# Kernel optimization log

Measured on AMD Instinct MI355X. Metric: run time of the kernel, lower is better.

## Reference

```python
import jax, jax.numpy as jnp
import numpy as np

EPS = 1e-5
NEG_SLOPE = 0.1


def setup_inputs() -> dict:
    key = jax.random.key(0)
    ks = jax.random.split(key, 4)
    B, Cin, Cout, D, E, EMB = 2, 32, 32, 40, 3, 1
    return {
        "x": jax.random.normal(ks[0], (B, Cin, D, D, D), dtype=jnp.float32),
        "embedding": jax.random.normal(ks[1], (B, EMB), dtype=jnp.float32),
        "route_w": jax.random.normal(ks[2], (EMB, E), dtype=jnp.float32),
        "route_b": jnp.zeros((E,), dtype=jnp.float32),
        "expert_kernels": jax.random.normal(ks[3], (E, Cout, Cin, 3, 3, 3), dtype=jnp.float32) * 0.05,
        "expert_bias": jnp.zeros((E, Cout), dtype=jnp.float32),
        "gamma": jnp.ones((Cout,), dtype=jnp.float32),
        "beta": jnp.zeros((Cout,), dtype=jnp.float32),
    }


def reference(x, embedding, route_w, route_b, expert_kernels, expert_bias, gamma, beta):
    # CondConv routing: sigmoid(Linear(embedding)) -> per-sample expert weights [B, E]
    r = jax.nn.sigmoid(embedding @ route_w + route_b)
    # Per-sample combined kernel [B, O, I, 3, 3, 3] and bias [B, O]
    w = jnp.einsum('be,eoixyz->boixyz', r, expert_kernels)
    b = r @ expert_bias

    def conv_one(xi, wi):
        # xi: [Cin, D, H, W], wi: [O, I, 3, 3, 3] -> [Cout, D, H, W]
        return jax.lax.conv_general_dilated(
            xi[None], wi, window_strides=(1, 1, 1), padding='SAME',
            dimension_numbers=('NCDHW', 'OIDHW', 'NCDHW'))[0]

    y = jax.vmap(conv_one)(x, w) + b[:, :, None, None, None]  # [B, O, D, H, W]

    # BatchNorm3d (training mode: biased batch stats over B,D,H,W per channel)
    mean = jnp.mean(y, axis=(0, 2, 3, 4), keepdims=True)
    var = jnp.mean(jnp.square(y - mean), axis=(0, 2, 3, 4), keepdims=True)
    y = (y - mean) * jax.lax.rsqrt(var + EPS)
    y = y * gamma[None, :, None, None, None] + beta[None, :, None, None, None]

    # LeakyReLU(0.1)
    y = jnp.where(y >= 0, y, NEG_SLOPE * y)

    # Upsample nearest, scale_factor=2 on all 3 spatial dims
    y = jnp.repeat(jnp.repeat(jnp.repeat(y, 2, axis=2), 2, axis=3), 2, axis=4)
    return y
```

## Files before the change

### kernel.cpp

```cpp
#include <hip/hip_runtime.h>
#include <hip/hip_bf16.h>
#include <math.h>

#define BB   2
#define CIN  32
#define COUT 32
#define DM   40
#define PD   42
#define NPTS (DM*DM)
#define NVOL (DM*DM*DM)
#define EPSBN 1e-5f
#define NSLOT 64

typedef short  bf16x8  __attribute__((ext_vector_type(8)));
typedef short  bf16x4  __attribute__((ext_vector_type(4)));
typedef float  floatx4 __attribute__((ext_vector_type(4)));

#define WS_WFRAG 0
#define WS_BCOMB 27648
#define WS_SUM2  27712
#define WS_XPAD2 31808
#define WS_Y     2402624

#define REPACK_BLOCKS (PD*PD*BB)
#define NW_ELEMS  (2*2*27*64*8)
#define PREP_ELEMS (NW_ELEMS + 64 + NSLOT*64)
#define PREP_BLOCKS ((PREP_ELEMS + 255) / 256)

static __device__ __forceinline__ short f2bf(float f) {
    __hip_bfloat16 h = __float2bfloat16(f);
    return *reinterpret_cast<short*>(&h);
}
static __device__ __forceinline__ float bf2f(short s) {
    union { unsigned u; float f; } cv;
    cv.u = ((unsigned)(unsigned short)s) << 16;
    return cv.f;
}

__global__ void prep_repack_kernel(const float* __restrict__ x,
                                   const float* __restrict__ emb,
                                   const float* __restrict__ rw,
                                   const float* __restrict__ rb,
                                   const float* __restrict__ ek,
                                   const float* __restrict__ ebias,
                                   float* __restrict__ ws) {
    __shared__ __hip_bfloat16 tile[PD * 32];
    const int bid = blockIdx.x;
    const int t = threadIdx.x;
    if (bid < REPACK_BLOCKS) {
        int b  = bid / (PD * PD);
        int r  = bid % (PD * PD);
        int zp = r / PD, yp = r % PD;
        __hip_bfloat16* row = (__hip_bfloat16*)(ws + WS_XPAD2) +
                              ((((size_t)b * PD + zp) * PD + yp) * PD) * 32;
        const bool inz = (zp >= 1 && zp <= DM && yp >= 1 && yp <= DM);
        const int i  = t >> 3;
        const int xl = t & 7;
        #pragma unroll
        for (int k = 0; k < 6; ++k) {
            int xp = xl + 8 * k;
            if (xp < PD) {
                float v = 0.0f;
                if (inz && xp >= 1 && xp <= DM)
                    v = x[(size_t)(b * CIN + i) * NVOL +
                          (zp - 1) * NPTS + (yp - 1) * DM + (xp - 1)];
                tile[xp * 32 + i] = __float2bfloat16(v);
            }
        }
        __syncthreads();
        const unsigned* ts = (const unsigned*)tile;
        unsigned* rowu = (unsigned*)row;
        for (int j = t; j < PD * 32 / 2; j += 256) rowu[j] = ts[j];
        return;
    }
    int idx = (bid - REPACK_BLOCKS) * 256 + t;
    __hip_bfloat16* wfrag = (__hip_bfloat16*)(ws + WS_WFRAG);
    if (idx < NW_ELEMS) {
        int j    = idx & 7;
        int lane = (idx >> 3) & 63;
        int tap  = (idx >> 9) % 27;
        int nt   = (idx / (27 * 512)) & 1;
        int b    = idx / (2 * 27 * 512);
        int o = nt * 16 + (lane & 15);
        int i = (lane >> 4) * 8 + j;
        float e0 = emb[b];
        float w = 0.0f;
        #pragma unroll
        for (int e = 0; e < 3; ++e) {
            float r = 1.0f / (1.0f + expf(-(e0 * rw[e] + rb[e])));
            w += r * ek[((e * COUT + o) * CIN + i) * 27 + tap];
        }
        wfrag[idx] = __float2bfloat16(w);
    } else if (idx < NW_ELEMS + 64) {
        int j2 = idx - NW_ELEMS;
        int b = j2 >> 5, o = j2 & 31;
        float e0 = emb[b];
        float bv = 0.0f;
        #pragma unroll
        for (int e = 0; e < 3; ++e) {
            float r = 1.0f / (1.0f + expf(-(e0 * rw[e] + rb[e])));
            bv += r * ebias[e * COUT + o];
        }
        ws[WS_BCOMB + j2] = bv;
    } else if (idx < PREP_ELEMS) {
        ws[WS_SUM2 + (idx - NW_ELEMS - 64)] = 0.0f;
    }
}

__global__ __launch_bounds__(256, 8) void conv_mfma_kernel(
        const __hip_bfloat16* __restrict__ xp2,
        const bf16x8* __restrict__ wfrag,
        const float* __restrict__ bcomb,
        __hip_bfloat16* __restrict__ y,
        float* __restrict__ sums2) {
    const int g   = blockIdx.x & 7;
    const int s   = blockIdx.x >> 3;
    const int b   = s / 125;
    const int rem = s % 125;
    const int z   = g * 5 + rem / 25;
    const int mc  = rem % 25;

    const int tid = threadIdx.x, lane = tid & 63, wv = tid >> 6;
    const int mt = wv & 1, nt = wv >> 1;
    const int quad = lane >> 4, l15 = lane & 15;

    __shared__ float lstat[64];
    __shared__ short ytile[32 * 72];
    __shared__ short atile[5 * PD * 32];

    if (tid < 64) lstat[tid] = 0.0f;

    const int y0  = (mc * 64) / DM;
    const int pa0 = mc * 64 + mt * 32 + l15;
    const int pa1 = pa0 + 16;
    const int ya0 = pa0 / DM, xa0 = pa0 % DM;
    const int ya1 = pa1 / DM, xa1 = pa1 % DM;
    const int af0 = ((ya0 - y0) * PD + xa0) * 32 + quad * 8;
    const int af1 = ((ya1 - y0) * PD + xa1) * 32 + quad * 8;

    const bf16x8* wbase = wfrag + ((b * 2 + nt) * 27) * 64 + lane;
    const int nrows = min(5, PD - y0);
    const int nchunk = nrows * (PD * 32 / 8);

    floatx4 acc0 = {0.f, 0.f, 0.f, 0.f};
    floatx4 acc1 = {0.f, 0.f, 0.f, 0.f};

    for (int dz = 0; dz < 3; ++dz) {
        __syncthreads();
        {
            const bf16x8* src = (const bf16x8*)(xp2 +
                ((((size_t)b * PD + (z + dz)) * PD + y0) * PD) * 32);
            bf16x8* dst = (bf16x8*)atile;
            for (int j = tid; j < nchunk; j += 256) dst[j] = src[j];
        }
        __syncthreads();
        #pragma unroll
        for (int t9 = 0; t9 < 9; ++t9) {
            const int dy = t9 / 3, dx = t9 % 3;
            const int aoff = (dy * PD + dx) * 32;
            bf16x8 av0 = *(const bf16x8*)&atile[af0 + aoff];
            bf16x8 av1 = *(const bf16x8*)&atile[af1 + aoff];
            bf16x8 bv  = wbase[(dz * 9 + t9) * 64];
            acc0 = __builtin_amdgcn_mfma_f32_16x16x32_bf16(av0, bv, acc0, 0, 0, 0);
            acc1 = __builtin_amdgcn_mfma_f32_16x16x32_bf16(av1, bv, acc1, 0, 0, 0);
        }
    }

    const int o = nt * 16 + l15;
    const float bias = bcomb[b * COUT + o];

    float u0 = acc0[0] + bias, u1 = acc0[1] + bias;
    float u2 = acc0[2] + bias, u3 = acc0[3] + bias;
    float w0 = acc1[0] + bias, w1 = acc1[1] + bias;
    float w2 = acc1[2] + bias, w3 = acc1[3] + bias;

    {
        const int s0 = mt * 32 + quad * 4;
        bf16x4 p0 = { f2bf(u0), f2bf(u1), f2bf(u2), f2bf(u3) };
        bf16x4 p1 = { f2bf(w0), f2bf(w1), f2bf(w2), f2bf(w3) };
        *(bf16x4*)&ytile[o * 72 + s0]      = p0;
        *(bf16x4*)&ytile[o * 72 + s0 + 16] = p1;
    }

    float vs = u0 + u1 + u2 + u3 + w0 + w1 + w2 + w3;
    float vq = u0*u0 + u1*u1 + u2*u2 + u3*u3 + w0*w0 + w1*w1 + w2*w2 + w3*w3;
    vs += __shfl_xor(vs, 16); vq += __shfl_xor(vq, 16);
    vs += __shfl_xor(vs, 32); vq += __shfl_xor(vq, 32);
    if (lane < 16) {
        atomicAdd(&lstat[o],      vs);
        atomicAdd(&lstat[32 + o], vq);
    }
    __syncthreads();

    {
        const int o2 = tid >> 3, c = tid & 7;
        bf16x8 v = *(const bf16x8*)&ytile[o2 * 72 + c * 8];
        __hip_bfloat16* dst = y + ((size_t)(b * COUT + o2) * DM + z) * NPTS
                            + mc * 64 + c * 8;
        *(bf16x8*)dst = v;
    }
    if (tid < 64) {
        int slot = ((b * DM + z) * 25 + mc) & (NSLOT - 1);
        atomicAdd(&sums2[slot * 64 + tid], lstat[tid]);
    }
}

__global__ __launch_bounds__(256) void upsample_kernel(
        const __hip_bfloat16* __restrict__ yin,
        const float* __restrict__ sums2,
        const float* __restrict__ gamma,
        const float* __restrict__ beta,
        float* __restrict__ out) {
    __shared__ float partl[4][64];
    __shared__ float ssc[32], ssh[32];
    __shared__ float fplane[NPTS];
    const int tid = threadIdx.x;
    const int cc  = blockIdx.x / DM;
    const int z   = blockIdx.x % DM;
    const int c   = cc & 31;

    {
        int sg = tid >> 6, st = tid & 63;
        float p = 0.0f;
        #pragma unroll
        for (int s = 0; s < 16; ++s) p += sums2[(sg * 16 + s) * 64 + st];
        partl[sg][st] = p;
    }
    __syncthreads();
    if (tid < 64) {
        partl[0][tid] += partl[1][tid] + partl[2][tid] + partl[3][tid];
    }
    __syncthreads();
    if (tid < 32) {
        const float invN = 1.0f / (float)(BB * NVOL);
        float mean  = partl[0][tid] * invN;
        float var   = partl[0][32 + tid] * invN - mean * mean;
        float scale = gamma[tid] * rsqrtf(var + EPSBN);
        ssc[tid] = scale;
        ssh[tid] = beta[tid] - mean * scale;
    }
    __syncthreads();

    const float sc = ssc[c], sh = ssh[c];
    if (tid < NPTS / 8) {
        bf16x8 rv = *(const bf16x8*)(yin + ((size_t)cc * DM + z) * NPTS + tid * 8);
        #pragma unroll
        for (int j = 0; j < 8; ++j) {
            float v = bf2f(rv[j]) * sc + sh;
            fplane[tid * 8 + j] = (v >= 0.0f) ? v : 0.1f * v;
        }
    }
    __syncthreads();

    float* outp = out + ((size_t)cc * 80 + 2 * z) * 6400;
    #pragma unroll 2
    for (int cch = tid; cch < 2 * 1600; cch += 256) {
        int plane = cch / 1600;
        int cp    = cch - plane * 1600;
        int yy2   = cp / 20;
        int sx0   = (cp % 20) * 2;
        const float* srow = fplane + (yy2 >> 1) * DM;
        float v0 = srow[sx0], v1 = srow[sx0 + 1];
        floatx4 q = {v0, v0, v1, v1};
        *(floatx4*)(outp + (size_t)plane * 6400 + cp * 4) = q;
    }
}

extern "C" void kernel_launch(void* const* d_in, const int* in_sizes, int n_in,
                              void* d_out, int out_size, void* d_ws, size_t ws_size,
                              hipStream_t stream) {
    const float* x     = (const float*)d_in[0];
    const float* emb   = (const float*)d_in[1];
    const float* rw    = (const float*)d_in[2];
    const float* rb    = (const float*)d_in[3];
    const float* ek    = (const float*)d_in[4];
    const float* ebias = (const float*)d_in[5];
    const float* gamma = (const float*)d_in[6];
    const float* beta  = (const float*)d_in[7];
    float* ws  = (float*)d_ws;
    float* out = (float*)d_out;

    prep_repack_kernel<<<REPACK_BLOCKS + PREP_BLOCKS, 256, 0, stream>>>(
        x, emb, rw, rb, ek, ebias, ws);

    conv_mfma_kernel<<<2000, 256, 0, stream>>>(
        (const __hip_bfloat16*)(ws + WS_XPAD2), (const bf16x8*)(ws + WS_WFRAG),
        ws + WS_BCOMB, (__hip_bfloat16*)(ws + WS_Y), ws + WS_SUM2);

    upsample_kernel<<<BB * COUT * DM, 256, 0, stream>>>(
        (const __hip_bfloat16*)(ws + WS_Y), ws + WS_SUM2, gamma, beta, out);
}
```

Before: 179.5 us.

## Swizzle conv LDS tile to avoid bank conflicts and reorder repack blocks

The activation tile copied into LDS is now stored with an XOR swizzle on the 16-byte chunk index, and the MFMA operand reads use the matching swizzled addresses. The aim is to cut LDS bank conflicts on the bf16x8 fragment loads. The repack grid is also remapped so that block indices interleave eight z-groups. This likely matches the z-slab order the conv kernel consumes, improving locality or overlap, at the cost of some idle blocks that return early.

```diff
diff --git a/kernel.cpp b/kernel.cpp
--- a/kernel.cpp
+++ b/kernel.cpp
@@ -22,7 +22,7 @@
 #define WS_XPAD2 31808
 #define WS_Y     2402624
 
-#define REPACK_BLOCKS (PD*PD*BB)
+#define REPACK_GRID (8 * 504)
 #define NW_ELEMS  (2*2*27*64*8)
 #define PREP_ELEMS (NW_ELEMS + 64 + NSLOT*64)
 #define PREP_BLOCKS ((PREP_ELEMS + 255) / 256)
@@ -47,18 +47,25 @@
     __shared__ __hip_bfloat16 tile[PD * 32];
     const int bid = blockIdx.x;
     const int t = threadIdx.x;
-    if (bid < REPACK_BLOCKS) {
-        int b  = bid / (PD * PD);
-        int r  = bid % (PD * PD);
-        int zp = r / PD, yp = r % PD;
+    if (bid < REPACK_GRID) {
+        const int g  = bid & 7;
+        const int k  = bid >> 3;
+        const int lz = k / (PD * BB);
+        const int rr = k % (PD * BB);
+        const int sz  = (g == 0 || g == 7) ? 6 : 5;
+        if (lz >= sz) return;
+        const int zlo = g ? 5 * g + 1 : 0;
+        const int zp = zlo + lz;
+        const int b  = rr / PD, yp = rr % PD;
+
         __hip_bfloat16* row = (__hip_bfloat16*)(ws + WS_XPAD2) +
                               ((((size_t)b * PD + zp) * PD + yp) * PD) * 32;
         const bool inz = (zp >= 1 && zp <= DM && yp >= 1 && yp <= DM);
         const int i  = t >> 3;
         const int xl = t & 7;
         #pragma unroll
-        for (int k = 0; k < 6; ++k) {
-            int xp = xl + 8 * k;
+        for (int kk = 0; kk < 6; ++kk) {
+            int xp = xl + 8 * kk;
             if (xp < PD) {
                 float v = 0.0f;
                 if (inz && xp >= 1 && xp <= DM)
@@ -73,7 +80,7 @@
         for (int j = t; j < PD * 32 / 2; j += 256) rowu[j] = ts[j];
         return;
     }
-    int idx = (bid - REPACK_BLOCKS) * 256 + t;
+    int idx = (bid - REPACK_GRID) * 256 + t;
     __hip_bfloat16* wfrag = (__hip_bfloat16*)(ws + WS_WFRAG);
     if (idx < NW_ELEMS) {
         int j    = idx & 7;
@@ -135,12 +142,12 @@
     const int pa1 = pa0 + 16;
     const int ya0 = pa0 / DM, xa0 = pa0 % DM;
     const int ya1 = pa1 / DM, xa1 = pa1 % DM;
-    const int af0 = ((ya0 - y0) * PD + xa0) * 32 + quad * 8;
-    const int af1 = ((ya1 - y0) * PD + xa1) * 32 + quad * 8;
+    const int cb0 = (ya0 - y0) * PD + xa0;
+    const int cb1 = (ya1 - y0) * PD + xa1;
 
     const bf16x8* wbase = wfrag + ((b * 2 + nt) * 27) * 64 + lane;
     const int nrows = min(5, PD - y0);
-    const int nchunk = nrows * (PD * 32 / 8);
+    const int nchunk = nrows * PD * 4;
 
     floatx4 acc0 = {0.f, 0.f, 0.f, 0.f};
     floatx4 acc1 = {0.f, 0.f, 0.f, 0.f};
@@ -151,15 +158,19 @@
             const bf16x8* src = (const bf16x8*)(xp2 +
                 ((((size_t)b * PD + (z + dz)) * PD + y0) * PD) * 32);
             bf16x8* dst = (bf16x8*)atile;
-            for (int j = tid; j < nchunk; j += 256) dst[j] = src[j];
+            for (int j = tid; j < nchunk; j += 256)
+                dst[j ^ ((j >> 3) & 3)] = src[j];
         }
         __syncthreads();
         #pragma unroll
         for (int t9 = 0; t9 < 9; ++t9) {
             const int dy = t9 / 3, dx = t9 % 3;
-            const int aoff = (dy * PD + dx) * 32;
-            bf16x8 av0 = *(const bf16x8*)&atile[af0 + aoff];
-            bf16x8 av1 = *(const bf16x8*)&atile[af1 + aoff];
+            const int c0 = cb0 + dy * PD + dx;
+            const int c1 = cb1 + dy * PD + dx;
+            const int p0 = c0 * 4 + (quad ^ ((c0 >> 1) & 3));
+            const int p1 = c1 * 4 + (quad ^ ((c1 >> 1) & 3));
+            bf16x8 av0 = *(const bf16x8*)&atile[p0 * 8];
+            bf16x8 av1 = *(const bf16x8*)&atile[p1 * 8];
             bf16x8 bv  = wbase[(dz * 9 + t9) * 64];
             acc0 = __builtin_amdgcn_mfma_f32_16x16x32_bf16(av0, bv, acc0, 0, 0, 0);
             acc1 = __builtin_amdgcn_mfma_f32_16x16x32_bf16(av1, bv, acc1, 0, 0, 0);
@@ -280,7 +291,7 @@
     float* ws  = (float*)d_ws;
     float* out = (float*)d_out;
 
-    prep_repack_kernel<<<REPACK_BLOCKS + PREP_BLOCKS, 256, 0, stream>>>(
+    prep_repack_kernel<<<REPACK_GRID + PREP_BLOCKS, 256, 0, stream>>>(
         x, emb, rw, rb, ek, ebias, ws);
 
     conv_mfma_kernel<<<2000, 256, 0, stream>>>(
```

New measurement: 186.2 us. +3.8%, slower.
